# Kernel tuning notes

Measured on AMD Instinct MI355X. Metric: run time of the kernel, lower is better.

The kernel has to match this reference:

```python
import jax, jax.numpy as jnp
import numpy as np

N_NODES = 65536
N_EDGES = 1048576


def gcn_conv(x, W, b, src, dst, n_nodes):
    """PyG GCNConv (normalize=True, add_self_loops already applied in src/dst):
    out = D^{-1/2} (A+I) D^{-1/2} X W + b, aggregated at dst (target) nodes."""
    deg = jax.ops.segment_sum(jnp.ones_like(dst, dtype=x.dtype), dst, num_segments=n_nodes)
    dis = jax.lax.rsqrt(jnp.maximum(deg, 1.0))  # self loops guarantee deg >= 1
    norm = dis[src] * dis[dst]                  # [E]
    h = x @ W                                   # [N, out]
    agg = jax.ops.segment_sum(h[src] * norm[:, None], dst, num_segments=n_nodes)
    return agg + b


def setup_inputs() -> dict:
    key = jax.random.key(0)
    ks = jax.random.split(key, 8)
    x = jax.random.normal(ks[0], (N_NODES, 128), dtype=jnp.float32)
    edge_index = jax.random.randint(ks[1], (2, N_EDGES), 0, N_NODES, dtype=jnp.int64)
    dims = [(128, 256), (256, 128), (128, 64)]
    params = {}
    for i, (din, dout) in enumerate(dims):
        scale = 1.0 / np.sqrt(din)
        params[f"W{i+1}"] = jax.random.uniform(ks[2 + i], (din, dout), dtype=jnp.float32, minval=-scale, maxval=scale)
        params[f"b{i+1}"] = jnp.zeros((dout,), dtype=jnp.float32)
    return {"x": x, "edge_index": edge_index, **params}


def reference(x, edge_index, W1, b1, W2, b2, W3, b3):
    n = x.shape[0]
    loop = jnp.arange(n, dtype=edge_index.dtype)
    src = jnp.concatenate([edge_index[0], loop])  # add self loops
    dst = jnp.concatenate([edge_index[1], loop])
    for W, b in ((W1, b1), (W2, b2), (W3, b3)):
        x = gcn_conv(x, W, b, src, dst, n)
        x = jax.nn.softmax(jax.nn.relu(x), axis=1)  # ReLU then Softmax(dim=1) per layer
    return x
```

## Files before the change

### kernel.cpp

```cpp
#include <hip/hip_runtime.h>
#include <cstdint>
#include <cstddef>

#define N_NODES 65536
#define N_EDGES 1048576
#define E_TOT   (N_EDGES + N_NODES)
#define CAP     5120

using short8  = __attribute__((ext_vector_type(8))) short;
using floatx4 = __attribute__((ext_vector_type(4))) float;
using half8   = __attribute__((ext_vector_type(8))) _Float16;
using half4   = __attribute__((ext_vector_type(4))) _Float16;
typedef unsigned short ushort_t;

__device__ inline void split_bf16(float a, short& hi, short& lo) {
    unsigned u  = __float_as_uint(a);
    unsigned hr = (u + 0x7fffu + ((u >> 16) & 1u)) >> 16;
    float    hf = __uint_as_float(hr << 16);
    hi = (short)hr;
    float    lf = a - hf;
    lo = (short)(__float_as_uint(lf) >> 16);
}


__global__ __launch_bounds__(1024) void k_bucket(const int* __restrict__ src, const int* __restrict__ dst,
                                                 int* __restrict__ gcur, unsigned* __restrict__ pk) {
    __shared__ int cnt[256];
    __shared__ int cur[256];
    int tid = threadIdx.x;
    if (tid < 256) cnt[tid] = 0;
    __syncthreads();
    int base = blockIdx.x * 4096;
    #pragma unroll
    for (int j = 0; j < 4; ++j) {
        int d = __builtin_nontemporal_load(&dst[base + j * 1024 + tid]);
        atomicAdd(&cnt[d >> 8], 1);
    }
    __syncthreads();
    if (tid < 256) cur[tid] = CAP * tid + atomicAdd(&gcur[tid], cnt[tid]);
    __syncthreads();
    #pragma unroll
    for (int j = 0; j < 4; ++j) {
        int e = base + j * 1024 + tid;
        int d = __builtin_nontemporal_load(&dst[e]);
        int s = __builtin_nontemporal_load(&src[e]);
        int pos = atomicAdd(&cur[d >> 8], 1);
        pk[pos] = ((unsigned)s << 16) | (unsigned)d;
    }
}

__global__ __launch_bounds__(256) void k_boff(const int* __restrict__ gcur, int* __restrict__ boff,
                                              int* __restrict__ off) {
    __shared__ int sb[256];
    int tid = threadIdx.x;
    int v = gcur[tid] + 256;
    sb[tid] = v;
    __syncthreads();
    #pragma unroll
    for (int s = 1; s < 256; s <<= 1) {
        int t = (tid >= s) ? sb[tid - s] : 0;
        __syncthreads();
        sb[tid] += t;
        __syncthreads();
    }
    boff[tid] = sb[tid] - v;
    if (tid == 255) boff[256] = sb[255];
    if (tid == 0) off[N_NODES] = E_TOT;
}

__global__ __launch_bounds__(1024) void k_sortb(const unsigned* __restrict__ pk, const int* __restrict__ gcur,
                                                const int* __restrict__ boff, int* __restrict__ off,
                                                float* __restrict__ dis, ushort_t* __restrict__ ssort) {
    __shared__ int cnt[256];
    __shared__ int sb[256];
    __shared__ int cur[256];
    int b = blockIdx.x;
    int tid = threadIdx.x;
    int n = gcur[b];
    const unsigned* p = pk + (size_t)b * CAP;
    if (tid < 256) cnt[tid] = 0;
    __syncthreads();
    for (int i = tid; i < n; i += 1024) atomicAdd(&cnt[p[i] & 255u], 1);
    __syncthreads();
    if (tid < 256) sb[tid] = cnt[tid];
    __syncthreads();
    #pragma unroll
    for (int s = 1; s < 256; s <<= 1) {
        int t = (tid < 256 && tid >= s) ? sb[tid - s] : 0;
        __syncthreads();
        if (tid < 256) sb[tid] += t;
        __syncthreads();
    }
    if (tid < 256) {
        int deg = cnt[tid];
        int o = boff[b] + (sb[tid] - deg) + tid;
        int d = b * 256 + tid;
        off[d] = o;
        dis[d] = rsqrtf((float)(deg + 1));
        ssort[o + deg] = (ushort_t)d;
        cur[tid] = o;
    }
    __syncthreads();
    for (int i = tid; i < n; i += 1024) {
        unsigned v = p[i];
        int pos = atomicAdd(&cur[v & 255u], 1);
        ssort[pos] = (ushort_t)(v >> 16);
    }
}


#define G1 (16 * 4 * 64)
#define G2 (8 * 8 * 64)
#define G3 (4 * 4 * 64)
#define NBX 8192
#define NBW ((G1 + G2 + G3 + 255) / 256)

__device__ inline void convw_split(const float* W, int K, int N, short* Bh, short* Bl, int g) {
    int lane = g & 63;
    int kt = (g >> 6) % (K / 32);
    int nt = (g >> 6) / (K / 32);
    int n = nt * 16 + (lane & 15);
    int kbase = kt * 32 + (lane >> 4) * 8;
    #pragma unroll
    for (int j = 0; j < 8; ++j) {
        short h, l;
        split_bf16(W[(size_t)(kbase + j) * N + n], h, l);
        Bh[(size_t)g * 8 + j] = h;
        Bl[(size_t)g * 8 + j] = l;
    }
}

__device__ inline void convw_h(const float* W, int K, int N, _Float16* Bf, int g) {
    int lane = g & 63;
    int kt = (g >> 6) % (K / 32);
    int nt = (g >> 6) / (K / 32);
    int n = nt * 16 + (lane & 15);
    int kbase = kt * 32 + (lane >> 4) * 8;
    #pragma unroll
    for (int j = 0; j < 8; ++j)
        Bf[(size_t)g * 8 + j] = (_Float16)W[(size_t)(kbase + j) * N + n];
}

__global__ __launch_bounds__(256) void k_fused(
        const float* __restrict__ x, const float* __restrict__ dis, _Float16* __restrict__ xh,
        const float* __restrict__ W1, short* __restrict__ w1h, short* __restrict__ w1l,
        const float* __restrict__ W2, _Float16* __restrict__ w2f,
        const float* __restrict__ W3, _Float16* __restrict__ w3f) {
    int b = blockIdx.x;
    if (b < NBX) {
        int idx = (b * 256 + threadIdx.x) * 4;
        int row = idx >> 7;
        float d = dis[row];
        float4 v = *(const float4*)(x + idx);
        half4 o = {(_Float16)(d * v.x), (_Float16)(d * v.y), (_Float16)(d * v.z), (_Float16)(d * v.w)};
        *(half4*)(xh + idx) = o;
    } else {
        int g = (b - NBX) * 256 + threadIdx.x;
        if (g < G1)                 convw_split(W1, 128, 256, w1h, w1l, g);
        else if (g < G1 + G2)       convw_h(W2, 256, 128, w2f, g - G1);
        else if (g < G1 + G2 + G3)  convw_h(W3, 128, 64, w3f, g - G1 - G2);
    }
}


__global__ __launch_bounds__(256) void k_l12(const _Float16* __restrict__ A,
        const short* __restrict__ Bh, const short* __restrict__ Bl,
        const float* __restrict__ b1,
        const _Float16* __restrict__ w2f,
        const float* __restrict__ dis, _Float16* __restrict__ hh) {
    constexpr int LSTR = 280;
    __shared__ __align__(16) _Float16 xt[64][LSTR];
    __shared__ float red[2][4][64];

    int tid = threadIdx.x;
    int w = tid >> 6, lane = tid & 63;
    int quad = lane >> 4, li = lane & 15;
    size_t row0 = (size_t)blockIdx.x * 64;

    floatx4 acc[4][4];
    #pragma unroll
    for (int ntl = 0; ntl < 4; ++ntl)
        #pragma unroll
        for (int rt = 0; rt < 4; ++rt) acc[ntl][rt] = (floatx4)0.0f;

    #pragma unroll
    for (int kt = 0; kt < 4; ++kt) {
        short8 afh[4], afl[4];
        #pragma unroll
        for (int rt = 0; rt < 4; ++rt) {
            half8 a8 = *(const half8*)(A + (row0 + rt * 16 + li) * 128 + kt * 32 + quad * 8);
            short ah[8], al[8];
            #pragma unroll
            for (int j = 0; j < 8; ++j) split_bf16((float)a8[j], ah[j], al[j]);
            afh[rt] = *(short8*)ah;
            afl[rt] = *(short8*)al;
        }
        #pragma unroll
        for (int ntl = 0; ntl < 4; ++ntl) {
            size_t bi = ((size_t)((w * 4 + ntl) * 4 + kt) * 64 + lane);
            short8 bfh = ((const short8*)Bh)[bi];
            short8 bfl = ((const short8*)Bl)[bi];
            #pragma unroll
            for (int rt = 0; rt < 4; ++rt) {
                acc[ntl][rt] = __builtin_amdgcn_mfma_f32_16x16x32_bf16(bfh, afh[rt], acc[ntl][rt], 0, 0, 0);
                acc[ntl][rt] = __builtin_amdgcn_mfma_f32_16x16x32_bf16(bfl, afh[rt], acc[ntl][rt], 0, 0, 0);
                acc[ntl][rt] = __builtin_amdgcn_mfma_f32_16x16x32_bf16(bfh, afl[rt], acc[ntl][rt], 0, 0, 0);
            }
        }
    }

    float bb[4][4];
    #pragma unroll
    for (int ntl = 0; ntl < 4; ++ntl) {
        float4 bv = *(const float4*)(b1 + w * 64 + ntl * 16 + quad * 4);
        bb[ntl][0] = bv.x; bb[ntl][1] = bv.y; bb[ntl][2] = bv.z; bb[ntl][3] = bv.w;
    }
    float mr[4] = {0.f, 0.f, 0.f, 0.f};
    #pragma unroll
    for (int ntl = 0; ntl < 4; ++ntl)
        #pragma unroll
        for (int rt = 0; rt < 4; ++rt)
            #pragma unroll
            for (int r = 0; r < 4; ++r) {
                float v = fmaxf(acc[ntl][rt][r] + bb[ntl][r], 0.0f);
                acc[ntl][rt][r] = v;
                mr[rt] = fmaxf(mr[rt], v);
            }
    #pragma unroll
    for (int rt = 0; rt < 4; ++rt) {
        mr[rt] = fmaxf(mr[rt], __shfl_xor(mr[rt], 16, 64));
        mr[rt] = fmaxf(mr[rt], __shfl_xor(mr[rt], 32, 64));
    }
    {
        float wv = (quad == 0) ? mr[0] : (quad == 1) ? mr[1] : (quad == 2) ? mr[2] : mr[3];
        red[0][w][quad * 16 + li] = wv;
    }
    __syncthreads();
    float m[4];
    #pragma unroll
    for (int rt = 0; rt < 4; ++rt) {
        int idx = rt * 16 + li;
        m[rt] = fmaxf(fmaxf(red[0][0][idx], red[0][1][idx]), fmaxf(red[0][2][idx], red[0][3][idx]));
    }
    float sr[4] = {0.f, 0.f, 0.f, 0.f};
    #pragma unroll
    for (int ntl = 0; ntl < 4; ++ntl)
        #pragma unroll
        for (int rt = 0; rt < 4; ++rt)
            #pragma unroll
            for (int r = 0; r < 4; ++r) {
                float t = __expf(acc[ntl][rt][r] - m[rt]);
                acc[ntl][rt][r] = t;
                sr[rt] += t;
            }
    #pragma unroll
    for (int rt = 0; rt < 4; ++rt) {
        sr[rt] += __shfl_xor(sr[rt], 16, 64);
        sr[rt] += __shfl_xor(sr[rt], 32, 64);
    }
    {
        float sv = (quad == 0) ? sr[0] : (quad == 1) ? sr[1] : (quad == 2) ? sr[2] : sr[3];
        red[1][w][quad * 16 + li] = sv;
    }
    __syncthreads();
    float inv[4];
    #pragma unroll
    for (int rt = 0; rt < 4; ++rt) {
        int idx = rt * 16 + li;
        inv[rt] = 1.0f / (red[1][0][idx] + red[1][1][idx] + red[1][2][idx] + red[1][3][idx]);
    }
    #pragma unroll
    for (int ntl = 0; ntl < 4; ++ntl)
        #pragma unroll
        for (int rt = 0; rt < 4; ++rt) {
            half4 h4 = {(_Float16)(acc[ntl][rt][0] * inv[rt]), (_Float16)(acc[ntl][rt][1] * inv[rt]),
                        (_Float16)(acc[ntl][rt][2] * inv[rt]), (_Float16)(acc[ntl][rt][3] * inv[rt])};
            *(half4*)(&xt[rt * 16 + li][w * 64 + ntl * 16 + quad * 4]) = h4;
        }
    __syncthreads();

    floatx4 acc2[2][4];
    #pragma unroll
    for (int ntl2 = 0; ntl2 < 2; ++ntl2)
        #pragma unroll
        for (int rt = 0; rt < 4; ++rt) acc2[ntl2][rt] = (floatx4)0.0f;

    #pragma unroll
    for (int kt = 0; kt < 8; ++kt) {
        half8 a8[4];
        #pragma unroll
        for (int rt = 0; rt < 4; ++rt)
            a8[rt] = *(const half8*)(&xt[rt * 16 + li][kt * 32 + quad * 8]);
        #pragma unroll
        for (int ntl2 = 0; ntl2 < 2; ++ntl2) {
            half8 bf = ((const half8*)w2f)[(size_t)((w * 2 + ntl2) * 8 + kt) * 64 + lane];
            #pragma unroll
            for (int rt = 0; rt < 4; ++rt)
                acc2[ntl2][rt] = __builtin_amdgcn_mfma_f32_16x16x32_f16(a8[rt], bf, acc2[ntl2][rt], 0, 0, 0);
        }
    }
    #pragma unroll
    for (int rt = 0; rt < 4; ++rt) {
        size_t rbase = row0 + rt * 16 + quad * 4;
        float4 d4 = *(const float4*)(dis + rbase);
        float dr[4] = {d4.x, d4.y, d4.z, d4.w};
        #pragma unroll
        for (int ntl2 = 0; ntl2 < 2; ++ntl2)
            #pragma unroll
            for (int r = 0; r < 4; ++r)
                hh[(rbase + r) * 128 + (w * 2 + ntl2) * 16 + li] = (_Float16)(acc2[ntl2][rt][r] * dr[r]);
    }
}


template <int K, int N>
__global__ __launch_bounds__(256) void k_mmh(const _Float16* __restrict__ A,
                                             const _Float16* __restrict__ Bf,
                                             const float* __restrict__ dis, _Float16* __restrict__ Cout) {
    constexpr int NT = N / 16;
    constexpr int KT = K / 32;
    int tid = threadIdx.x;
    int wave = tid >> 6, lane = tid & 63;
    int quad = lane >> 4, col = lane & 15;
    size_t row0 = (size_t)blockIdx.x * 64;
    const _Float16* ap = A + (row0 + wave * 16 + col) * K + quad * 8;

    floatx4 acc[NT];
    #pragma unroll
    for (int t = 0; t < NT; ++t) acc[t] = (floatx4)0.0f;

    for (int kt = 0; kt < KT; ++kt) {
        half8 a8 = *(const half8*)(ap + kt * 32);
        #pragma unroll
        for (int nt = 0; nt < NT; ++nt) {
            half8 bf = ((const half8*)Bf)[(size_t)(nt * KT + kt) * 64 + lane];
            acc[nt] = __builtin_amdgcn_mfma_f32_16x16x32_f16(a8, bf, acc[nt], 0, 0, 0);
        }
    }

    size_t rbase = row0 + wave * 16 + quad * 4;
    float4 d4 = *(const float4*)(dis + rbase);
    float dr[4] = {d4.x, d4.y, d4.z, d4.w};
    #pragma unroll
    for (int nt = 0; nt < NT; ++nt)
        #pragma unroll
        for (int r = 0; r < 4; ++r)
            Cout[(rbase + r) * N + nt * 16 + col] = (_Float16)(acc[nt][r] * dr[r]);
}


template <int LPN, bool ACT, typename OutT>
__global__ __launch_bounds__(256) void k_aggq(const _Float16* __restrict__ h, const int* __restrict__ off,
                                              const ushort_t* __restrict__ ss, const float* __restrict__ dis,
                                              const float* __restrict__ bias, OutT* __restrict__ out) {
    constexpr int D = LPN * 8;
    constexpr int NPW = 64 / LPN;
    int lane = threadIdx.x & 63;
    int grp  = lane / LPN;
    int li   = lane & (LPN - 1);
    int c0   = li * 8;
    int n = (blockIdx.x * 4 + (threadIdx.x >> 6)) * NPW + grp;
    int e0 = off[n], e1 = off[n + 1];

    const _Float16* hb = h + c0;

    half8 hacc = {0, 0, 0, 0, 0, 0, 0, 0};
    half8 hacc2 = {0, 0, 0, 0, 0, 0, 0, 0};
    float facc[8];
    #pragma unroll
    for (int j = 0; j < 8; ++j) facc[j] = 0.0f;

    int e = e0;
    for (; e + 8 <= e1; e += 8) {
        int s0 = ss[e];
        int s1 = ss[e + 1];
        int s2 = ss[e + 2];
        int s3 = ss[e + 3];
        int s4 = ss[e + 4];
        int s5 = ss[e + 5];
        int s6 = ss[e + 6];
        int s7 = ss[e + 7];
        half8 v0 = *(const half8*)(hb + (size_t)s0 * D);
        half8 v1 = *(const half8*)(hb + (size_t)s1 * D);
        half8 v2 = *(const half8*)(hb + (size_t)s2 * D);
        half8 v3 = *(const half8*)(hb + (size_t)s3 * D);
        half8 v4 = *(const half8*)(hb + (size_t)s4 * D);
        half8 v5 = *(const half8*)(hb + (size_t)s5 * D);
        half8 v6 = *(const half8*)(hb + (size_t)s6 * D);
        half8 v7 = *(const half8*)(hb + (size_t)s7 * D);
        half8 p0 = (v0 + v1) + (v2 + v3);
        half8 p1 = (v4 + v5) + (v6 + v7);
        if constexpr (ACT) {
            hacc  += p0;
            hacc2 += p1;
        } else {
            #pragma unroll
            for (int j = 0; j < 8; ++j) facc[j] += (float)p0[j];
            #pragma unroll
            for (int j = 0; j < 8; ++j) facc[j] += (float)p1[j];
        }
    }
    for (; e + 4 <= e1; e += 4) {
        int s0 = ss[e];
        int s1 = ss[e + 1];
        int s2 = ss[e + 2];
        int s3 = ss[e + 3];
        half8 v0 = *(const half8*)(hb + (size_t)s0 * D);
        half8 v1 = *(const half8*)(hb + (size_t)s1 * D);
        half8 v2 = *(const half8*)(hb + (size_t)s2 * D);
        half8 v3 = *(const half8*)(hb + (size_t)s3 * D);
        half8 p = (v0 + v1) + (v2 + v3);
        if constexpr (ACT) {
            hacc += p;
        } else {
            #pragma unroll
            for (int j = 0; j < 8; ++j) facc[j] += (float)p[j];
        }
    }
    int rem = e1 - e;
    if (rem > 0) {
        int s0 = ss[e];
        half8 p = *(const half8*)(hb + (size_t)s0 * D);
        if (rem > 1) {
            int s1 = ss[e + 1];
            p += *(const half8*)(hb + (size_t)s1 * D);
        }
        if (rem > 2) {
            int s2 = ss[e + 2];
            p += *(const half8*)(hb + (size_t)s2 * D);
        }
        if constexpr (ACT) {
            hacc += p;
        } else {
            #pragma unroll
            for (int j = 0; j < 8; ++j) facc[j] += (float)p[j];
        }
    }
    if constexpr (ACT) {
        hacc += hacc2;
        #pragma unroll
        for (int j = 0; j < 8; ++j) facc[j] = (float)hacc[j];
    }

    float dn = dis[n];
    if constexpr (ACT) {
        float m = 0.0f;
        #pragma unroll
        for (int j = 0; j < 8; ++j) {
            float v = fmaxf(fmaf(facc[j], dn, bias[c0 + j]), 0.0f);
            facc[j] = v;
            m = fmaxf(m, v);
        }
        #pragma unroll
        for (int mask = LPN / 2; mask > 0; mask >>= 1) m = fmaxf(m, __shfl_xor(m, mask, 64));
        float sum = 0.0f;
        #pragma unroll
        for (int j = 0; j < 8; ++j) {
            float t = __expf(facc[j] - m);
            facc[j] = t;
            sum += t;
        }
        #pragma unroll
        for (int mask = LPN / 2; mask > 0; mask >>= 1) sum += __shfl_xor(sum, mask, 64);
        float inv = 1.0f / sum;
        #pragma unroll
        for (int j = 0; j < 8; ++j) facc[j] *= inv;
    } else {
        #pragma unroll
        for (int j = 0; j < 8; ++j) facc[j] *= dn;
    }

    if constexpr (sizeof(OutT) == 2) {
        half8 o;
        #pragma unroll
        for (int j = 0; j < 8; ++j) o[j] = (_Float16)facc[j];
        *(half8*)((_Float16*)out + (size_t)n * D + c0) = o;
    } else {
        float* op = (float*)out + (size_t)n * D + c0;
        *(float4*)(op)     = make_float4(facc[0], facc[1], facc[2], facc[3]);
        *(float4*)(op + 4) = make_float4(facc[4], facc[5], facc[6], facc[7]);
    }
}


extern "C" void kernel_launch(void* const* d_in, const int* in_sizes, int n_in,
                              void* d_out, int out_size, void* d_ws, size_t ws_size,
                              hipStream_t stream) {
    const float* x  = (const float*)d_in[0];
    const int*   ei = (const int*)d_in[1];
    const float* W1 = (const float*)d_in[2];
    const float* b1 = (const float*)d_in[3];
    const float* W2 = (const float*)d_in[4];
    const float* b2 = (const float*)d_in[5];
    const float* W3 = (const float*)d_in[6];
    const float* b3 = (const float*)d_in[7];
    const int* srcE = ei;
    const int* dstE = ei + N_EDGES;

    char* p = (char*)d_ws;
    auto carve = [&](size_t bytes) {
        char* q = p;
        p += (bytes + 255) & ~(size_t)255;
        return q;
    };
    int*          gcur  = (int*)carve(sizeof(int) * 256);
    int*          boff  = (int*)carve(sizeof(int) * 257);
    int*          off   = (int*)carve(sizeof(int) * (N_NODES + 1));
    float*        dis   = (float*)carve(sizeof(float) * N_NODES);
    unsigned*     pk    = (unsigned*)carve(sizeof(unsigned) * 256 * CAP);
    ushort_t*     ssort = (ushort_t*)carve(sizeof(ushort_t) * E_TOT);
    short*        w1h   = (short*)carve(sizeof(short) * 128 * 256);
    short*        w1l   = (short*)carve(sizeof(short) * 128 * 256);
    _Float16*     w2f   = (_Float16*)carve(sizeof(_Float16) * 256 * 128);
    _Float16*     w3f   = (_Float16*)carve(sizeof(_Float16) * 128 * 64);
    _Float16*     xh    = (_Float16*)carve(sizeof(_Float16) * (size_t)N_NODES * 128);
    _Float16*     a0h   = (_Float16*)carve(sizeof(_Float16) * (size_t)N_NODES * 128);
    _Float16*     x2h   = (_Float16*)carve(sizeof(_Float16) * (size_t)N_NODES * 128);
    _Float16*     hh    = (_Float16*)carve(sizeof(_Float16) * (size_t)N_NODES * 128);

    (void)hipMemsetAsync(gcur, 0, sizeof(int) * 256, stream);
    k_bucket<<<256, 1024, 0, stream>>>(srcE, dstE, gcur, pk);
    k_boff<<<1, 256, 0, stream>>>(gcur, boff, off);
    k_sortb<<<256, 1024, 0, stream>>>(pk, gcur, boff, off, dis, ssort);
    k_fused<<<NBX + NBW, 256, 0, stream>>>(x, dis, xh, W1, w1h, w1l, W2, w2f, W3, w3f);

    k_aggq<16, false, _Float16><<<N_NODES / 16, 256, 0, stream>>>(xh, off, ssort, dis, nullptr, a0h);
    k_l12<<<N_NODES / 64, 256, 0, stream>>>(a0h, w1h, w1l, b1, w2f, dis, hh);
    k_aggq<16, true, _Float16><<<N_NODES / 16, 256, 0, stream>>>(hh, off, ssort, dis, b2, x2h);
    k_mmh<128, 64><<<N_NODES / 64, 256, 0, stream>>>(x2h, w3f, dis, hh);
    k_aggq<8, true, float><<<N_NODES / 32, 256, 0, stream>>>(hh, off, ssort, dis, b3, (float*)d_out);
}
```

Before: 254.2 us.

## Split aggregation into column slices and move activations into downstream kernels

The gather-aggregation kernels now split the feature dimension into 8 column slices, one per block, so each pass gathers a narrower slice of every neighbour row. The aim is to shrink the working set per pass and improve L2 hit rates on the random source gathers. The ReLU+softmax of layer 2 moves into the layer-3 matmul kernel's prologue, and layer 3's activation moves into a separate small kernel. In exchange the neighbour index lists are read once per slice, the FP16 accumulation of raw sums may lose precision, and an extra kernel launch plus intermediate buffer are added.

```diff
diff --git a/kernel.cpp b/kernel.cpp
--- a/kernel.cpp
+++ b/kernel.cpp
@@ -313,56 +313,94 @@
 }
 
 
-template <int K, int N>
-__global__ __launch_bounds__(256) void k_mmh(const _Float16* __restrict__ A,
-                                             const _Float16* __restrict__ Bf,
-                                             const float* __restrict__ dis, _Float16* __restrict__ Cout) {
-    constexpr int NT = N / 16;
-    constexpr int KT = K / 32;
+__global__ __launch_bounds__(256) void k_mmh3(const _Float16* __restrict__ Araw,
+                                              const _Float16* __restrict__ Bf,
+                                              const float* __restrict__ dis, const float* __restrict__ b2,
+                                              _Float16* __restrict__ Cout) {
     int tid = threadIdx.x;
     int wave = tid >> 6, lane = tid & 63;
     int quad = lane >> 4, col = lane & 15;
     size_t row0 = (size_t)blockIdx.x * 64;
-    const _Float16* ap = A + (row0 + wave * 16 + col) * K + quad * 8;
-
-    floatx4 acc[NT];
-    #pragma unroll
-    for (int t = 0; t < NT; ++t) acc[t] = (floatx4)0.0f;
-
-    for (int kt = 0; kt < KT; ++kt) {
-        half8 a8 = *(const half8*)(ap + kt * 32);
-        #pragma unroll
-        for (int nt = 0; nt < NT; ++nt) {
-            half8 bf = ((const half8*)Bf)[(size_t)(nt * KT + kt) * 64 + lane];
-            acc[nt] = __builtin_amdgcn_mfma_f32_16x16x32_f16(a8, bf, acc[nt], 0, 0, 0);
-        }
-    }
+    size_t arow = row0 + wave * 16 + col;
+    const _Float16* ap = Araw + arow * 128 + quad * 8;
+
+    half8 a8[4];
+    #pragma unroll
+    for (int kt = 0; kt < 4; ++kt) a8[kt] = *(const half8*)(ap + kt * 32);
+
+    float dn = dis[arow];
+    float v[4][8];
+    float m = 0.0f;
+    #pragma unroll
+    for (int kt = 0; kt < 4; ++kt) {
+        int c0 = kt * 32 + quad * 8;
+        float4 bv0 = *(const float4*)(b2 + c0);
+        float4 bv1 = *(const float4*)(b2 + c0 + 4);
+        float bb[8] = {bv0.x, bv0.y, bv0.z, bv0.w, bv1.x, bv1.y, bv1.z, bv1.w};
+        #pragma unroll
+        for (int j = 0; j < 8; ++j) {
+            float t = fmaxf(fmaf((float)a8[kt][j], dn, bb[j]), 0.0f);
+            v[kt][j] = t;
+            m = fmaxf(m, t);
+        }
+    }
+    m = fmaxf(m, __shfl_xor(m, 16, 64));
+    m = fmaxf(m, __shfl_xor(m, 32, 64));
+    float sum = 0.0f;
+    #pragma unroll
+    for (int kt = 0; kt < 4; ++kt)
+        #pragma unroll
+        for (int j = 0; j < 8; ++j) {
+            float t = __expf(v[kt][j] - m);
+            v[kt][j] = t;
+            sum += t;
+        }
+    sum += __shfl_xor(sum, 16, 64);
+    sum += __shfl_xor(sum, 32, 64);
+    float inv = 1.0f / sum;
+    #pragma unroll
+    for (int kt = 0; kt < 4; ++kt)
+        #pragma unroll
+        for (int j = 0; j < 8; ++j) a8[kt][j] = (_Float16)(v[kt][j] * inv);
+
+    floatx4 acc[4];
+    #pragma unroll
+    for (int t = 0; t < 4; ++t) acc[t] = (floatx4)0.0f;
+    #pragma unroll
+    for (int kt = 0; kt < 4; ++kt)
+        #pragma unroll
+        for (int nt = 0; nt < 4; ++nt) {
+            half8 bf = ((const half8*)Bf)[(size_t)(nt * 4 + kt) * 64 + lane];
+            acc[nt] = __builtin_amdgcn_mfma_f32_16x16x32_f16(a8[kt], bf, acc[nt], 0, 0, 0);
+        }
 
     size_t rbase = row0 + wave * 16 + quad * 4;
     float4 d4 = *(const float4*)(dis + rbase);
     float dr[4] = {d4.x, d4.y, d4.z, d4.w};
     #pragma unroll
-    for (int nt = 0; nt < NT; ++nt)
+    for (int nt = 0; nt < 4; ++nt)
         #pragma unroll
         for (int r = 0; r < 4; ++r)
-            Cout[(rbase + r) * N + nt * 16 + col] = (_Float16)(acc[nt][r] * dr[r]);
-}
-
-
-template <int LPN, bool ACT, typename OutT>
-__global__ __launch_bounds__(256) void k_aggq(const _Float16* __restrict__ h, const int* __restrict__ off,
-                                              const ushort_t* __restrict__ ss, const float* __restrict__ dis,
-                                              const float* __restrict__ bias, OutT* __restrict__ out) {
-    constexpr int D = LPN * 8;
+            Cout[(rbase + r) * 64 + nt * 16 + col] = (_Float16)(acc[nt][r] * dr[r]);
+}
+
+
+template <int D, bool FACC>
+__global__ __launch_bounds__(256) void k_aggcs(const _Float16* __restrict__ h, const int* __restrict__ off,
+                                               const ushort_t* __restrict__ ss, const float* __restrict__ dis,
+                                               _Float16* __restrict__ out) {
+    constexpr int W = D / 8;
+    constexpr int LPN = W / 8;
     constexpr int NPW = 64 / LPN;
+    int slice = blockIdx.x & 7;
+    int chunk = blockIdx.x >> 3;
     int lane = threadIdx.x & 63;
+    int li   = (LPN == 1) ? 0 : (lane & (LPN - 1));
     int grp  = lane / LPN;
-    int li   = lane & (LPN - 1);
-    int c0   = li * 8;
-    int n = (blockIdx.x * 4 + (threadIdx.x >> 6)) * NPW + grp;
+    int n = (chunk * 4 + (threadIdx.x >> 6)) * NPW + grp;
     int e0 = off[n], e1 = off[n + 1];
 
-    const _Float16* hb = h + c0;
+    const _Float16* hb = h + slice * W + li * 8;
 
     half8 hacc = {0, 0, 0, 0, 0, 0, 0, 0};
     half8 hacc2 = {0, 0, 0, 0, 0, 0, 0, 0};
@@ -390,14 +428,14 @@
         half8 v7 = *(const half8*)(hb + (size_t)s7 * D);
         half8 p0 = (v0 + v1) + (v2 + v3);
         half8 p1 = (v4 + v5) + (v6 + v7);
-        if constexpr (ACT) {
+        if constexpr (FACC) {
+            #pragma unroll
+            for (int j = 0; j < 8; ++j) facc[j] += (float)p0[j];
+            #pragma unroll
+            for (int j = 0; j < 8; ++j) facc[j] += (float)p1[j];
+        } else {
             hacc  += p0;
             hacc2 += p1;
-        } else {
-            #pragma unroll
-            for (int j = 0; j < 8; ++j) facc[j] += (float)p0[j];
-            #pragma unroll
-            for (int j = 0; j < 8; ++j) facc[j] += (float)p1[j];
         }
     }
     for (; e + 4 <= e1; e += 4) {
@@ -410,11 +448,11 @@
         half8 v2 = *(const half8*)(hb + (size_t)s2 * D);
         half8 v3 = *(const half8*)(hb + (size_t)s3 * D);
         half8 p = (v0 + v1) + (v2 + v3);
-        if constexpr (ACT) {
+        if constexpr (FACC) {
+            #pragma unroll
+            for (int j = 0; j < 8; ++j) facc[j] += (float)p[j];
+        } else {
             hacc += p;
-        } else {
-            #pragma unroll
-            for (int j = 0; j < 8; ++j) facc[j] += (float)p[j];
         }
     }
     int rem = e1 - e;
@@ -429,57 +467,57 @@
             int s2 = ss[e + 2];
             p += *(const half8*)(hb + (size_t)s2 * D);
         }
-        if constexpr (ACT) {
+        if constexpr (FACC) {
+            #pragma unroll
+            for (int j = 0; j < 8; ++j) facc[j] += (float)p[j];
+        } else {
             hacc += p;
-        } else {
-            #pragma unroll
-            for (int j = 0; j < 8; ++j) facc[j] += (float)p[j];
-        }
-    }
-    if constexpr (ACT) {
+        }
+    }
+
+    half8 o;
+    if constexpr (FACC) {
+        float dn = dis[n];
+        #pragma unroll
+        for (int j = 0; j < 8; ++j) o[j] = (_Float16)(facc[j] * dn);
+    } else {
         hacc += hacc2;
-        #pragma unroll
-        for (int j = 0; j < 8; ++j) facc[j] = (float)hacc[j];
-    }
-
+        o = hacc;
+    }
+    *(half8*)(out + (size_t)n * D + slice * W + li * 8) = o;
+}
+
+
+__global__ __launch_bounds__(256) void k_act64(const _Float16* __restrict__ raw, const float* __restrict__ dis,
+                                               const float* __restrict__ b3, float* __restrict__ out) {
+    int lane = threadIdx.x & 63;
+    int li = lane & 7, grp = lane >> 3;
+    int n = (blockIdx.x * 4 + (threadIdx.x >> 6)) * 8 + grp;
+    half8 r = *(const half8*)(raw + (size_t)n * 64 + li * 8);
     float dn = dis[n];
-    if constexpr (ACT) {
-        float m = 0.0f;
-        #pragma unroll
-        for (int j = 0; j < 8; ++j) {
-            float v = fmaxf(fmaf(facc[j], dn, bias[c0 + j]), 0.0f);
-            facc[j] = v;
-            m = fmaxf(m, v);
-        }
-        #pragma unroll
-        for (int mask = LPN / 2; mask > 0; mask >>= 1) m = fmaxf(m, __shfl_xor(m, mask, 64));
-        float sum = 0.0f;
-        #pragma unroll
-        for (int j = 0; j < 8; ++j) {
-            float t = __expf(facc[j] - m);
-            facc[j] = t;
-            sum += t;
-        }
-        #pragma unroll
-        for (int mask = LPN / 2; mask > 0; mask >>= 1) sum += __shfl_xor(sum, mask, 64);
-        float inv = 1.0f / sum;
-        #pragma unroll
-        for (int j = 0; j < 8; ++j) facc[j] *= inv;
-    } else {
-        #pragma unroll
-        for (int j = 0; j < 8; ++j) facc[j] *= dn;
-    }
-
-    if constexpr (sizeof(OutT) == 2) {
-        half8 o;
-        #pragma unroll
-        for (int j = 0; j < 8; ++j) o[j] = (_Float16)facc[j];
-        *(half8*)((_Float16*)out + (size_t)n * D + c0) = o;
-    } else {
-        float* op = (float*)out + (size_t)n * D + c0;
-        *(float4*)(op)     = make_float4(facc[0], facc[1], facc[2], facc[3]);
-        *(float4*)(op + 4) = make_float4(facc[4], facc[5], facc[6], facc[7]);
-    }
+    float facc[8];
+    float m = 0.0f;
+    #pragma unroll
+    for (int j = 0; j < 8; ++j) {
+        float vv = fmaxf(fmaf((float)r[j], dn, b3[li * 8 + j]), 0.0f);
+        facc[j] = vv;
+        m = fmaxf(m, vv);
+    }
+    #pragma unroll
+    for (int mask = 4; mask > 0; mask >>= 1) m = fmaxf(m, __shfl_xor(m, mask, 64));
+    float sum = 0.0f;
+    #pragma unroll
+    for (int j = 0; j < 8; ++j) {
+        float t = __expf(facc[j] - m);
+        facc[j] = t;
+        sum += t;
+    }
+    #pragma unroll
+    for (int mask = 4; mask > 0; mask >>= 1) sum += __shfl_xor(sum, mask, 64);
+    float inv = 1.0f / sum;
+    float* op = out + (size_t)n * 64 + li * 8;
+    *(float4*)(op)     = make_float4(facc[0] * inv, facc[1] * inv, facc[2] * inv, facc[3] * inv);
+    *(float4*)(op + 4) = make_float4(facc[4] * inv, facc[5] * inv, facc[6] * inv, facc[7] * inv);
 }
 
 
@@ -515,8 +553,9 @@
     _Float16*     w3f   = (_Float16*)carve(sizeof(_Float16) * 128 * 64);
     _Float16*     xh    = (_Float16*)carve(sizeof(_Float16) * (size_t)N_NODES * 128);
     _Float16*     a0h   = (_Float16*)carve(sizeof(_Float16) * (size_t)N_NODES * 128);
-    _Float16*     x2h   = (_Float16*)carve(sizeof(_Float16) * (size_t)N_NODES * 128);
+    _Float16*     x2r   = (_Float16*)carve(sizeof(_Float16) * (size_t)N_NODES * 128);
     _Float16*     hh    = (_Float16*)carve(sizeof(_Float16) * (size_t)N_NODES * 128);
+    _Float16*     o3r   = (_Float16*)carve(sizeof(_Float16) * (size_t)N_NODES * 64);
 
     (void)hipMemsetAsync(gcur, 0, sizeof(int) * 256, stream);
     k_bucket<<<256, 1024, 0, stream>>>(srcE, dstE, gcur, pk);
@@ -524,9 +563,10 @@
     k_sortb<<<256, 1024, 0, stream>>>(pk, gcur, boff, off, dis, ssort);
     k_fused<<<NBX + NBW, 256, 0, stream>>>(x, dis, xh, W1, w1h, w1l, W2, w2f, W3, w3f);
 
-    k_aggq<16, false, _Float16><<<N_NODES / 16, 256, 0, stream>>>(xh, off, ssort, dis, nullptr, a0h);
+    k_aggcs<128, true><<<(N_NODES / 128) * 8, 256, 0, stream>>>(xh, off, ssort, dis, a0h);
     k_l12<<<N_NODES / 64, 256, 0, stream>>>(a0h, w1h, w1l, b1, w2f, dis, hh);
-    k_aggq<16, true, _Float16><<<N_NODES / 16, 256, 0, stream>>>(hh, off, ssort, dis, b2, x2h);
-    k_mmh<128, 64><<<N_NODES / 64, 256, 0, stream>>>(x2h, w3f, dis, hh);
-    k_aggq<8, true, float><<<N_NODES / 32, 256, 0, stream>>>(hh, off, ssort, dis, b3, (float*)d_out);
-}
+    k_aggcs<128, false><<<(N_NODES / 128) * 8, 256, 0, stream>>>(hh, off, ssort, dis, x2r);
+    k_mmh3<<<N_NODES / 64, 256, 0, stream>>>(x2r, w3f, dis, b2, hh);
+    k_aggcs<64, false><<<(N_NODES / 256) * 8, 256, 0, stream>>>(hh, off, ssort, dis, o3r);
+    k_act64<<<N_NODES / 32, 256, 0, stream>>>(o3r, dis, b3, (float*)d_out);
+}
```

Result: slower. 480.8 us (+89.1%).

## Emit bf16 hi/lo split from layer-1 aggregation and widen k_l12 to 512 threads

Applied to the files above, without the earlier changes.

The first aggregation kernel now applies dis scaling and splits its result directly into bf16 hi and lo arrays, so k_l12 loads pre-split operands instead of converting fp16 to a bf16 pair per element. k_l12 moves from 4 to 8 waves per block, each wave covering half as many output tiles in both GEMMs, which cuts per-thread accumulators and register pressure. The row softmax reduction now combines 8 wave partials. The trade is doubled intermediate storage and traffic for a0 (two short arrays instead of one half array) and the same A fragments being loaded by twice as many waves. Keeping the layer-1 aggregate in fp32 before splitting, rather than rounding to fp16 first, may also change numerics slightly.

```diff
diff --git a/kernel.cpp b/kernel.cpp
--- a/kernel.cpp
+++ b/kernel.cpp
@@ -163,23 +163,23 @@
 }
 
 
-__global__ __launch_bounds__(256) void k_l12(const _Float16* __restrict__ A,
+__global__ __launch_bounds__(512) void k_l12(const short* __restrict__ Ahi, const short* __restrict__ Alo,
         const short* __restrict__ Bh, const short* __restrict__ Bl,
         const float* __restrict__ b1,
         const _Float16* __restrict__ w2f,
         const float* __restrict__ dis, _Float16* __restrict__ hh) {
     constexpr int LSTR = 280;
     __shared__ __align__(16) _Float16 xt[64][LSTR];
-    __shared__ float red[2][4][64];
+    __shared__ float red[2][8][64];
 
     int tid = threadIdx.x;
     int w = tid >> 6, lane = tid & 63;
     int quad = lane >> 4, li = lane & 15;
     size_t row0 = (size_t)blockIdx.x * 64;
 
-    floatx4 acc[4][4];
-    #pragma unroll
-    for (int ntl = 0; ntl < 4; ++ntl)
+    floatx4 acc[2][4];
+    #pragma unroll
+    for (int ntl = 0; ntl < 2; ++ntl)
         #pragma unroll
         for (int rt = 0; rt < 4; ++rt) acc[ntl][rt] = (floatx4)0.0f;
 
@@ -188,16 +188,13 @@
         short8 afh[4], afl[4];
         #pragma unroll
         for (int rt = 0; rt < 4; ++rt) {
-            half8 a8 = *(const half8*)(A + (row0 + rt * 16 + li) * 128 + kt * 32 + quad * 8);
-            short ah[8], al[8];
-            #pragma unroll
-            for (int j = 0; j < 8; ++j) split_bf16((float)a8[j], ah[j], al[j]);
-            afh[rt] = *(short8*)ah;
-            afl[rt] = *(short8*)al;
-        }
-        #pragma unroll
-        for (int ntl = 0; ntl < 4; ++ntl) {
-            size_t bi = ((size_t)((w * 4 + ntl) * 4 + kt) * 64 + lane);
+            size_t ao = (row0 + rt * 16 + li) * 128 + kt * 32 + quad * 8;
+            afh[rt] = *(const short8*)(Ahi + ao);
+            afl[rt] = *(const short8*)(Alo + ao);
+        }
+        #pragma unroll
+        for (int ntl = 0; ntl < 2; ++ntl) {
+            size_t bi = ((size_t)((w * 2 + ntl) * 4 + kt) * 64 + lane);
             short8 bfh = ((const short8*)Bh)[bi];
             short8 bfl = ((const short8*)Bl)[bi];
             #pragma unroll
@@ -209,15 +206,15 @@
         }
     }
 
-    float bb[4][4];
-    #pragma unroll
-    for (int ntl = 0; ntl < 4; ++ntl) {
-        float4 bv = *(const float4*)(b1 + w * 64 + ntl * 16 + quad * 4);
+    float bb[2][4];
+    #pragma unroll
+    for (int ntl = 0; ntl < 2; ++ntl) {
+        float4 bv = *(const float4*)(b1 + (w * 2 + ntl) * 16 + quad * 4);
         bb[ntl][0] = bv.x; bb[ntl][1] = bv.y; bb[ntl][2] = bv.z; bb[ntl][3] = bv.w;
     }
     float mr[4] = {0.f, 0.f, 0.f, 0.f};
     #pragma unroll
-    for (int ntl = 0; ntl < 4; ++ntl)
+    for (int ntl = 0; ntl < 2; ++ntl)
         #pragma unroll
         for (int rt = 0; rt < 4; ++rt)
             #pragma unroll
@@ -240,11 +237,15 @@
     #pragma unroll
     for (int rt = 0; rt < 4; ++rt) {
         int idx = rt * 16 + li;
-        m[rt] = fmaxf(fmaxf(red[0][0][idx], red[0][1][idx]), fmaxf(red[0][2][idx], red[0][3][idx]));
+        float m01 = fmaxf(red[0][0][idx], red[0][1][idx]);
+        float m23 = fmaxf(red[0][2][idx], red[0][3][idx]);
+        float m45 = fmaxf(red[0][4][idx], red[0][5][idx]);
+        float m67 = fmaxf(red[0][6][idx], red[0][7][idx]);
+        m[rt] = fmaxf(fmaxf(m01, m23), fmaxf(m45, m67));
     }
     float sr[4] = {0.f, 0.f, 0.f, 0.f};
     #pragma unroll
-    for (int ntl = 0; ntl < 4; ++ntl)
+    for (int ntl = 0; ntl < 2; ++ntl)
         #pragma unroll
         for (int rt = 0; rt < 4; ++rt)
             #pragma unroll
@@ -267,23 +268,23 @@
     #pragma unroll
     for (int rt = 0; rt < 4; ++rt) {
         int idx = rt * 16 + li;
-        inv[rt] = 1.0f / (red[1][0][idx] + red[1][1][idx] + red[1][2][idx] + red[1][3][idx]);
-    }
-    #pragma unroll
-    for (int ntl = 0; ntl < 4; ++ntl)
+        float s = ((red[1][0][idx] + red[1][1][idx]) + (red[1][2][idx] + red[1][3][idx]))
+                + ((red[1][4][idx] + red[1][5][idx]) + (red[1][6][idx] + red[1][7][idx]));
+        inv[rt] = 1.0f / s;
+    }
+    #pragma unroll
+    for (int ntl = 0; ntl < 2; ++ntl)
         #pragma unroll
         for (int rt = 0; rt < 4; ++rt) {
             half4 h4 = {(_Float16)(acc[ntl][rt][0] * inv[rt]), (_Float16)(acc[ntl][rt][1] * inv[rt]),
                         (_Float16)(acc[ntl][rt][2] * inv[rt]), (_Float16)(acc[ntl][rt][3] * inv[rt])};
-            *(half4*)(&xt[rt * 16 + li][w * 64 + ntl * 16 + quad * 4]) = h4;
-        }
-    __syncthreads();
-
-    floatx4 acc2[2][4];
-    #pragma unroll
-    for (int ntl2 = 0; ntl2 < 2; ++ntl2)
-        #pragma unroll
-        for (int rt = 0; rt < 4; ++rt) acc2[ntl2][rt] = (floatx4)0.0f;
+            *(half4*)(&xt[rt * 16 + li][(w * 2 + ntl) * 16 + quad * 4]) = h4;
+        }
+    __syncthreads();
+
+    floatx4 acc2[4];
+    #pragma unroll
+    for (int rt = 0; rt < 4; ++rt) acc2[rt] = (floatx4)0.0f;
 
     #pragma unroll
     for (int kt = 0; kt < 8; ++kt) {
@@ -291,13 +292,10 @@
         #pragma unroll
         for (int rt = 0; rt < 4; ++rt)
             a8[rt] = *(const half8*)(&xt[rt * 16 + li][kt * 32 + quad * 8]);
-        #pragma unroll
-        for (int ntl2 = 0; ntl2 < 2; ++ntl2) {
-            half8 bf = ((const half8*)w2f)[(size_t)((w * 2 + ntl2) * 8 + kt) * 64 + lane];
-            #pragma unroll
-            for (int rt = 0; rt < 4; ++rt)
-                acc2[ntl2][rt] = __builtin_amdgcn_mfma_f32_16x16x32_f16(a8[rt], bf, acc2[ntl2][rt], 0, 0, 0);
-        }
+        half8 bf = ((const half8*)w2f)[(size_t)(w * 8 + kt) * 64 + lane];
+        #pragma unroll
+        for (int rt = 0; rt < 4; ++rt)
+            acc2[rt] = __builtin_amdgcn_mfma_f32_16x16x32_f16(a8[rt], bf, acc2[rt], 0, 0, 0);
     }
     #pragma unroll
     for (int rt = 0; rt < 4; ++rt) {
@@ -305,10 +303,8 @@
         float4 d4 = *(const float4*)(dis + rbase);
         float dr[4] = {d4.x, d4.y, d4.z, d4.w};
         #pragma unroll
-        for (int ntl2 = 0; ntl2 < 2; ++ntl2)
-            #pragma unroll
-            for (int r = 0; r < 4; ++r)
-                hh[(rbase + r) * 128 + (w * 2 + ntl2) * 16 + li] = (_Float16)(acc2[ntl2][rt][r] * dr[r]);
+        for (int r = 0; r < 4; ++r)
+            hh[(rbase + r) * 128 + w * 16 + li] = (_Float16)(acc2[rt][r] * dr[r]);
     }
 }
 
@@ -349,10 +345,11 @@
 }
 
 
-template <int LPN, bool ACT, typename OutT>
+template <int LPN, int OM, typename OutT>
 __global__ __launch_bounds__(256) void k_aggq(const _Float16* __restrict__ h, const int* __restrict__ off,
                                               const ushort_t* __restrict__ ss, const float* __restrict__ dis,
-                                              const float* __restrict__ bias, OutT* __restrict__ out) {
+                                              const float* __restrict__ bias, OutT* __restrict__ out,
+                                              short* __restrict__ oh, short* __restrict__ ol) {
     constexpr int D = LPN * 8;
     constexpr int NPW = 64 / LPN;
     int lane = threadIdx.x & 63;
@@ -390,7 +387,7 @@
         half8 v7 = *(const half8*)(hb + (size_t)s7 * D);
         half8 p0 = (v0 + v1) + (v2 + v3);
         half8 p1 = (v4 + v5) + (v6 + v7);
-        if constexpr (ACT) {
+        if constexpr (OM != 0) {
             hacc  += p0;
             hacc2 += p1;
         } else {
@@ -410,7 +407,7 @@
         half8 v2 = *(const half8*)(hb + (size_t)s2 * D);
         half8 v3 = *(const half8*)(hb + (size_t)s3 * D);
         half8 p = (v0 + v1) + (v2 + v3);
-        if constexpr (ACT) {
+        if constexpr (OM != 0) {
             hacc += p;
         } else {
             #pragma unroll
@@ -429,46 +426,50 @@
             int s2 = ss[e + 2];
             p += *(const half8*)(hb + (size_t)s2 * D);
         }
-        if constexpr (ACT) {
+        if constexpr (OM != 0) {
             hacc += p;
         } else {
             #pragma unroll
             for (int j = 0; j < 8; ++j) facc[j] += (float)p[j];
         }
     }
-    if constexpr (ACT) {
+    if constexpr (OM != 0) {
         hacc += hacc2;
         #pragma unroll
         for (int j = 0; j < 8; ++j) facc[j] = (float)hacc[j];
     }
 
     float dn = dis[n];
-    if constexpr (ACT) {
-        float m = 0.0f;
-        #pragma unroll
-        for (int j = 0; j < 8; ++j) {
-            float v = fmaxf(fmaf(facc[j], dn, bias[c0 + j]), 0.0f);
-            facc[j] = v;
-            m = fmaxf(m, v);
-        }
-        #pragma unroll
-        for (int mask = LPN / 2; mask > 0; mask >>= 1) m = fmaxf(m, __shfl_xor(m, mask, 64));
-        float sum = 0.0f;
-        #pragma unroll
-        for (int j = 0; j < 8; ++j) {
-            float t = __expf(facc[j] - m);
-            facc[j] = t;
-            sum += t;
-        }
-        #pragma unroll
-        for (int mask = LPN / 2; mask > 0; mask >>= 1) sum += __shfl_xor(sum, mask, 64);
-        float inv = 1.0f / sum;
-        #pragma unroll
-        for (int j = 0; j < 8; ++j) facc[j] *= inv;
-    } else {
-        #pragma unroll
-        for (int j = 0; j < 8; ++j) facc[j] *= dn;
-    }
+    if constexpr (OM == 0) {
+        short hi[8], lo[8];
+        #pragma unroll
+        for (int j = 0; j < 8; ++j) split_bf16(facc[j] * dn, hi[j], lo[j]);
+        *(short8*)(oh + (size_t)n * D + c0) = *(short8*)hi;
+        *(short8*)(ol + (size_t)n * D + c0) = *(short8*)lo;
+        return;
+    }
+
+    float m = 0.0f;
+    #pragma unroll
+    for (int j = 0; j < 8; ++j) {
+        float v = fmaxf(fmaf(facc[j], dn, bias[c0 + j]), 0.0f);
+        facc[j] = v;
+        m = fmaxf(m, v);
+    }
+    #pragma unroll
+    for (int mask = LPN / 2; mask > 0; mask >>= 1) m = fmaxf(m, __shfl_xor(m, mask, 64));
+    float sum = 0.0f;
+    #pragma unroll
+    for (int j = 0; j < 8; ++j) {
+        float t = __expf(facc[j] - m);
+        facc[j] = t;
+        sum += t;
+    }
+    #pragma unroll
+    for (int mask = LPN / 2; mask > 0; mask >>= 1) sum += __shfl_xor(sum, mask, 64);
+    float inv = 1.0f / sum;
+    #pragma unroll
+    for (int j = 0; j < 8; ++j) facc[j] *= inv;
 
     if constexpr (sizeof(OutT) == 2) {
         half8 o;
@@ -514,7 +515,8 @@
     _Float16*     w2f   = (_Float16*)carve(sizeof(_Float16) * 256 * 128);
     _Float16*     w3f   = (_Float16*)carve(sizeof(_Float16) * 128 * 64);
     _Float16*     xh    = (_Float16*)carve(sizeof(_Float16) * (size_t)N_NODES * 128);
-    _Float16*     a0h   = (_Float16*)carve(sizeof(_Float16) * (size_t)N_NODES * 128);
+    short*        a0hi  = (short*)carve(sizeof(short) * (size_t)N_NODES * 128);
+    short*        a0lo  = (short*)carve(sizeof(short) * (size_t)N_NODES * 128);
     _Float16*     x2h   = (_Float16*)carve(sizeof(_Float16) * (size_t)N_NODES * 128);
     _Float16*     hh    = (_Float16*)carve(sizeof(_Float16) * (size_t)N_NODES * 128);
 
@@ -524,9 +526,10 @@
     k_sortb<<<256, 1024, 0, stream>>>(pk, gcur, boff, off, dis, ssort);
     k_fused<<<NBX + NBW, 256, 0, stream>>>(x, dis, xh, W1, w1h, w1l, W2, w2f, W3, w3f);
 
-    k_aggq<16, false, _Float16><<<N_NODES / 16, 256, 0, stream>>>(xh, off, ssort, dis, nullptr, a0h);
-    k_l12<<<N_NODES / 64, 256, 0, stream>>>(a0h, w1h, w1l, b1, w2f, dis, hh);
-    k_aggq<16, true, _Float16><<<N_NODES / 16, 256, 0, stream>>>(hh, off, ssort, dis, b2, x2h);
+    k_aggq<16, 0, _Float16><<<N_NODES / 16, 256, 0, stream>>>(xh, off, ssort, dis, nullptr,
+                                                              (_Float16*)nullptr, a0hi, a0lo);
+    k_l12<<<N_NODES / 64, 512, 0, stream>>>(a0hi, a0lo, w1h, w1l, b1, w2f, dis, hh);
+    k_aggq<16, 1, _Float16><<<N_NODES / 16, 256, 0, stream>>>(hh, off, ssort, dis, b2, x2h, nullptr, nullptr);
     k_mmh<128, 64><<<N_NODES / 64, 256, 0, stream>>>(x2h, w3f, dis, hh);
-    k_aggq<8, true, float><<<N_NODES / 32, 256, 0, stream>>>(hh, off, ssort, dis, b3, (float*)d_out);
-}
+    k_aggq<8, 2, float><<<N_NODES / 32, 256, 0, stream>>>(hh, off, ssort, dis, b3, (float*)d_out, nullptr, nullptr);
+}
```

New measurement: 270.5 us. +6.4%, slower.
